# Optimization experiments

Hardware: AMD Instinct MI355X
Metric: run time of the kernel (lower is better)

The kernel has to match this reference:

```python
import jax, jax.numpy as jnp
import numpy as np

N, L = 32, 2048
C_S, C_E, C_H, K, NRES = 384, 32, 128, 7, 20
C_IN = C_S + C_E  # 416
EPS = 1e-8


def setup_inputs() -> dict:
    key = jax.random.key(0)
    ks = jax.random.split(key, 32)
    s = 0.02
    d = {}
    d['aa_seq'] = jax.random.randint(ks[0], (L,), 0, NRES)
    d['sfea_tns'] = jax.random.normal(ks[1], (N, L, C_S), jnp.float32)
    d['sfea_tns_init'] = jax.random.normal(ks[2], (N, L, C_S), jnp.float32)
    d['encd_tns'] = jax.random.normal(ks[3], (N, L, C_E), jnp.float32)
    d['quat_tns'] = jax.random.normal(ks[4], (N, L, 4), jnp.float32)
    d['trsl_tns'] = jax.random.normal(ks[5], (N, L, 3), jnp.float32)
    # FrameHead linears
    d['Wq'] = jax.random.normal(ks[6], (C_IN, 4), jnp.float32) * s
    d['bq'] = jnp.zeros((4,), jnp.float32)
    d['Wt'] = jax.random.normal(ks[7], (C_IN, 3), jnp.float32) * s
    d['bt'] = jnp.zeros((3,), jnp.float32)
    # 20 per-residue-type AngleHead experts, stacked on leading axis
    d['Wa1'] = jax.random.normal(ks[8], (NRES, C_IN, C_H), jnp.float32) * s
    d['ba1'] = jnp.zeros((NRES, C_H), jnp.float32)
    d['Wa2'] = jax.random.normal(ks[9], (NRES, C_IN, C_H), jnp.float32) * s
    d['ba2'] = jnp.zeros((NRES, C_H), jnp.float32)
    d['Wb1a'] = jax.random.normal(ks[10], (NRES, C_H, C_H), jnp.float32) * s
    d['bb1a'] = jnp.zeros((NRES, C_H), jnp.float32)
    d['Wb1b'] = jax.random.normal(ks[11], (NRES, C_H, C_H), jnp.float32) * s
    d['bb1b'] = jnp.zeros((NRES, C_H), jnp.float32)
    d['Wb2a'] = jax.random.normal(ks[12], (NRES, C_H, C_H), jnp.float32) * s
    d['bb2a'] = jnp.zeros((NRES, C_H), jnp.float32)
    d['Wb2b'] = jax.random.normal(ks[13], (NRES, C_H, C_H), jnp.float32) * s
    d['bb2b'] = jnp.zeros((NRES, C_H), jnp.float32)
    d['Wout'] = jax.random.normal(ks[14], (NRES, C_H, K * 2), jnp.float32) * s
    d['bout'] = jnp.zeros((NRES, K * 2), jnp.float32)
    return d


def _qnorm(q):
    return q * jax.lax.rsqrt(jnp.sum(q * q, -1, keepdims=True) + EPS)


def _quat_mul(q, p):
    w1, x1, y1, z1 = jnp.split(q, 4, -1)
    w2, x2, y2, z2 = jnp.split(p, 4, -1)
    return jnp.concatenate([
        w1 * w2 - x1 * x2 - y1 * y2 - z1 * z2,
        w1 * x2 + x1 * w2 + y1 * z2 - z1 * y2,
        w1 * y2 - x1 * z2 + y1 * w2 + z1 * x2,
        w1 * z2 + x1 * y2 - y1 * x2 + z1 * w2], -1)


def _quat_rotate(q, v):
    # rotate vector v by unit quaternion q = (w, xyz)
    w, qv = q[..., :1], q[..., 1:]
    t = 2.0 * jnp.cross(qv, v)
    return v + w * t + jnp.cross(qv, t)


def _angle_net(sfcd, sfcd_init, aa, Wa1, ba1, Wa2, ba2,
               Wb1a, bb1a, Wb1b, bb1b, Wb2a, bb2a, Wb2b, bb2b, Wout, bout):
    # residue-type routed AngleHead: gather each token's expert weights by aa index
    g = lambda W: jnp.take(W, aa, axis=0)  # [L, ...]
    relu = jax.nn.relu
    a = (jnp.einsum('nlc,lch->nlh', relu(sfcd), g(Wa1)) + g(ba1)
         + jnp.einsum('nlc,lch->nlh', relu(sfcd_init), g(Wa2)) + g(ba2))
    # residual block 1
    h = jnp.einsum('nlh,lhk->nlk', relu(a), g(Wb1a)) + g(bb1a)
    a = a + jnp.einsum('nlh,lhk->nlk', relu(h), g(Wb1b)) + g(bb1b)
    # residual block 2
    h = jnp.einsum('nlh,lhk->nlk', relu(a), g(Wb2a)) + g(bb2a)
    a = a + jnp.einsum('nlh,lhk->nlk', relu(h), g(Wb2b)) + g(bb2b)
    out = jnp.einsum('nlh,lhk->nlk', relu(a), g(Wout)) + g(bout)  # [N,L,2K]
    ang = out.reshape(out.shape[0], out.shape[1], K, 2)
    norm = jnp.sqrt(jnp.sum(ang * ang, -1, keepdims=True) + 1e-12)
    return ang / norm


def reference(aa_seq, sfea_tns, sfea_tns_init, encd_tns, quat_tns, trsl_tns,
              Wq, bq, Wt, bt, Wa1, ba1, Wa2, ba2, Wb1a, bb1a, Wb1b, bb1b,
              Wb2a, bb2a, Wb2b, bb2b, Wout, bout):
    sfcd = jnp.concatenate([sfea_tns, encd_tns], -1)          # [N,L,C_IN]
    sfcd_init = jnp.concatenate([sfea_tns_init, encd_tns], -1)
    # FrameHead: quaternion/translation update signals
    quat_upd = sfcd @ Wq + bq                                  # [N,L,4]
    trsl_upd = sfcd @ Wt + bt                                  # [N,L,3]
    q_old = _qnorm(quat_tns)
    quat_new = _qnorm(_quat_mul(q_old, _qnorm(quat_upd)))
    trsl_new = trsl_tns + _quat_rotate(q_old, trsl_upd)
    angl_tns = _angle_net(sfcd, sfcd_init, aa_seq, Wa1, ba1, Wa2, ba2,
                          Wb1a, bb1a, Wb1b, bb1b, Wb2a, bb2a, Wb2b, bb2b,
                          Wout, bout)
    return quat_new, trsl_new, angl_tns, quat_upd
```

## Files before the change

### kernel.cpp

```cpp
#include <hip/hip_runtime.h>

#define L_SEQ 2048
#define CS 384
#define CE 32
#define CIN 416
#define CH 128
#define NRES 20

#define ABST 136

#define PERM_BYTES 8192
#define WA_PER (CH*CIN)
#define WB_PER (CH*CH)
#define WO_PER (16*CH)
#define OFF_WA1T 0
#define OFF_WA2T (NRES*WA_PER)
#define OFF_WB1AT (2*NRES*WA_PER)
#define OFF_WB1BT (OFF_WB1AT + 1*NRES*WB_PER)
#define OFF_WB2AT (OFF_WB1AT + 2*NRES*WB_PER)
#define OFF_WB2BT (OFF_WB1AT + 3*NRES*WB_PER)
#define OFF_WOUTT (OFF_WB1AT + 4*NRES*WB_PER)
#define TOTW (OFF_WOUTT + NRES*WO_PER)
#define WS_NEED ((size_t)PERM_BYTES + (size_t)4*TOTW)

#define OUT_TR 262144
#define OUT_ANG 458752
#define OUT_QU 1376256

#define LOSCALE 4096.0f
#define ILOSCALE (1.0f/4096.0f)
#define F16MIN 6.1035156e-5f

typedef _Float16 f16x8 __attribute__((ext_vector_type(8)));
typedef _Float16 f16x4 __attribute__((ext_vector_type(4)));
typedef float f32x4 __attribute__((ext_vector_type(4)));

#define MFMA16 __builtin_amdgcn_mfma_f32_16x16x32_f16

static __device__ __forceinline__ void split1(float x, _Float16& h, _Float16& l) {
  _Float16 hi = (__builtin_fabsf(x) < F16MIN) ? (_Float16)0.f : (_Float16)x;
  h = hi;
  l = (_Float16)((x - (float)hi) * LOSCALE);
}

static __device__ __forceinline__ void split8s(const float* x, f16x8& h, f16x8& l) {
  #pragma unroll
  for (int i = 0; i < 8; ++i) { _Float16 hh, ll; split1(x[i], hh, ll); h[i] = hh; l[i] = ll; }
}

static __device__ __forceinline__ void splitrelu4(const float4& v, f16x4& h, f16x4& l) {
  const float xs[4] = {v.x, v.y, v.z, v.w};
  #pragma unroll
  for (int i = 0; i < 4; ++i) {
    const float x = fmaxf(xs[i], 0.f);
    _Float16 hh, ll; split1(x, hh, ll); h[i] = hh; l[i] = ll;
  }
}

__global__ __launch_bounds__(256) void quat_head(
    const float* __restrict__ sfea, const float* __restrict__ encd,
    const float* __restrict__ quat, const float* __restrict__ trsl,
    const float* __restrict__ Wq, const float* __restrict__ bq,
    const float* __restrict__ Wt, const float* __restrict__ bt,
    float* __restrict__ out) {
  const int wv   = threadIdx.x >> 6;
  const int lane = threadIdx.x & 63;
  const size_t idx = (size_t)blockIdx.x * 4 + wv;
  const float* __restrict__ srow = sfea + idx * CS;

  float q0=0,q1=0,q2=0,q3=0,t0=0,t1=0,t2=0;
  #pragma unroll
  for (int cc = 0; cc < 6; ++cc) {
    const int ch = cc*64 + lane;
    const float s = srow[ch];
    const float4 wq = *reinterpret_cast<const float4*>(Wq + (size_t)ch*4);
    const float* wt = Wt + (size_t)ch*3;
    q0 += s*wq.x; q1 += s*wq.y; q2 += s*wq.z; q3 += s*wq.w;
    t0 += s*wt[0]; t1 += s*wt[1]; t2 += s*wt[2];
  }
  if (lane < CE) {
    const float s = encd[idx*CE + lane];
    const int ch = CS + lane;
    const float4 wq = *reinterpret_cast<const float4*>(Wq + (size_t)ch*4);
    const float* wt = Wt + (size_t)ch*3;
    q0 += s*wq.x; q1 += s*wq.y; q2 += s*wq.z; q3 += s*wq.w;
    t0 += s*wt[0]; t1 += s*wt[1]; t2 += s*wt[2];
  }
  #pragma unroll
  for (int off = 1; off < 64; off <<= 1) {
    q0 += __shfl_xor(q0, off); q1 += __shfl_xor(q1, off);
    q2 += __shfl_xor(q2, off); q3 += __shfl_xor(q3, off);
    t0 += __shfl_xor(t0, off); t1 += __shfl_xor(t1, off);
    t2 += __shfl_xor(t2, off);
  }
  if (lane == 0) {
    const float u0 = q0 + bq[0], u1 = q1 + bq[1], u2 = q2 + bq[2], u3 = q3 + bq[3];
    const float v0 = t0 + bt[0], v1 = t1 + bt[1], v2 = t2 + bt[2];
    float a0 = quat[idx*4+0], a1 = quat[idx*4+1], a2 = quat[idx*4+2], a3 = quat[idx*4+3];
    const float rq = rsqrtf(a0*a0+a1*a1+a2*a2+a3*a3 + 1e-8f);
    a0*=rq; a1*=rq; a2*=rq; a3*=rq;
    const float ru = rsqrtf(u0*u0+u1*u1+u2*u2+u3*u3 + 1e-8f);
    const float p0=u0*ru, p1=u1*ru, p2=u2*ru, p3=u3*ru;
    const float mw = a0*p0 - a1*p1 - a2*p2 - a3*p3;
    const float mx = a0*p1 + a1*p0 + a2*p3 - a3*p2;
    const float my = a0*p2 - a1*p3 + a2*p0 + a3*p1;
    const float mz = a0*p3 + a1*p2 - a2*p1 + a3*p0;
    const float rm = rsqrtf(mw*mw+mx*mx+my*my+mz*mz + 1e-8f);
    out[idx*4+0]=mw*rm; out[idx*4+1]=mx*rm; out[idx*4+2]=my*rm; out[idx*4+3]=mz*rm;
    const float tx = 2.f*(a2*v2 - a3*v1);
    const float ty = 2.f*(a3*v0 - a1*v2);
    const float tz = 2.f*(a1*v1 - a2*v0);
    out[OUT_TR + idx*3+0] = trsl[idx*3+0] + v0 + a0*tx + (a2*tz - a3*ty);
    out[OUT_TR + idx*3+1] = trsl[idx*3+1] + v1 + a0*ty + (a3*tx - a1*tz);
    out[OUT_TR + idx*3+2] = trsl[idx*3+2] + v2 + a0*tz + (a1*ty - a2*tx);
    out[OUT_QU + idx*4+0]=u0; out[OUT_QU + idx*4+1]=u1;
    out[OUT_QU + idx*4+2]=u2; out[OUT_QU + idx*4+3]=u3;
  }
}

__global__ __launch_bounds__(1024) void build_perm(const int* __restrict__ aa_seq,
                                                   int* __restrict__ perm) {
  __shared__ int cnt[NRES*32];
  __shared__ int off[NRES*32];
  const int t = threadIdx.x;
  const int wv = t >> 6, lane = t & 63;

  int aav[2];
  #pragma unroll
  for (int h = 0; h < 2; ++h) {
    const int W = wv + h*16;
    aav[h] = aa_seq[W*64 + lane];
    #pragma unroll
    for (int a = 0; a < NRES; ++a) {
      const unsigned long long m = __ballot(aav[h] == a);
      if (lane == a) cnt[a*32 + W] = (int)__popcll(m);
    }
  }
  __syncthreads();
  if (t < 64) {
    int carry = 0;
    #pragma unroll
    for (int c = 0; c < 10; ++c) {
      const int v0 = cnt[c*64 + t];
      int v = v0;
      #pragma unroll
      for (int o = 1; o < 64; o <<= 1) {
        const int u = __shfl_up(v, o);
        if (lane >= o) v += u;
      }
      off[c*64 + t] = carry + v - v0;
      carry += __shfl(v, 63);
    }
  }
  __syncthreads();
  const unsigned long long ltmask = (lane == 0) ? 0ull : (~0ull >> (64 - lane));
  #pragma unroll
  for (int h = 0; h < 2; ++h) {
    const int W = wv + h*16;
    const int aa = aav[h];
    int pos = 0;
    #pragma unroll
    for (int a = 0; a < NRES; ++a) {
      const unsigned long long m = __ballot(aa == a);
      if (aa == a) pos = off[a*32 + W] + (int)__popcll(m & ltmask);
    }
    perm[pos] = W*64 + lane;
  }
}

__global__ __launch_bounds__(256) void convert_w(
    const float* __restrict__ Wa1, const float* __restrict__ Wa2,
    const float* __restrict__ Wb1a, const float* __restrict__ Wb1b,
    const float* __restrict__ Wb2a, const float* __restrict__ Wb2b,
    const float* __restrict__ Wout, _Float16* __restrict__ wsw) {
  const int idx = blockIdx.x * 256 + threadIdx.x;
  if (idx >= TOTW) return;
  float v;
  if (idx < OFF_WB1AT) {
    const int which = (idx < OFF_WA2T) ? 0 : 1;
    const float* W = which ? Wa2 : Wa1;
    int r = idx - which * OFF_WA2T;
    const int aa = r / WA_PER; r -= aa * WA_PER;
    const int h = r / CIN;     const int c = r - h * CIN;
    v = W[((size_t)aa*CIN + c)*CH + h];
  } else if (idx < OFF_WOUTT) {
    int q = idx - OFF_WB1AT;
    const int which = q / (NRES*WB_PER);
    int r = q - which * (NRES*WB_PER);
    const float* W = (which==0)?Wb1a:(which==1)?Wb1b:(which==2)?Wb2a:Wb2b;
    const int aa = r / WB_PER; r -= aa * WB_PER;
    const int h = r / CH;      const int c = r - h * CH;
    v = W[((size_t)aa*CH + c)*CH + h];
  } else {
    int r = idx - OFF_WOUTT;
    const int aa = r / WO_PER; r -= aa * WO_PER;
    const int kk = r / CH;     const int c = r - kk * CH;
    v = (kk < 14) ? Wout[((size_t)aa*CH + c)*14 + kk] : 0.f;
  }
  _Float16 h, l; split1(v, h, l);
  wsw[idx] = h;
  wsw[(size_t)TOTW + idx] = l;
}

static __device__ __forceinline__ void bfrag_f32(const float* __restrict__ W, int rs,
                                                 int kbase, int col, f16x8& h, f16x8& l) {
  float x[8];
  const float* p = W + (size_t)kbase * rs + col;
  #pragma unroll
  for (int j = 0; j < 8; ++j) x[j] = p[(size_t)j * rs];
  split8s(x, h, l);
}

static __device__ __forceinline__ void fold(f32x4 acc[2][2], const f32x4 accL[2][2],
                                            float b0, float b1) {
  #pragma unroll
  for (int m = 0; m < 2; ++m)
    #pragma unroll
    for (int i = 0; i < 4; ++i) {
      acc[m][0][i] += accL[m][0][i]*ILOSCALE + b0;
      acc[m][1][i] += accL[m][1][i]*ILOSCALE + b1;
    }
}

static __device__ __forceinline__ void store_relu_pair(_Float16* dh, _Float16* dl,
    const f32x4 acc[2][2], int lane, int h0) {
  const int lr = lane & 15;
  const int r0 = (lane >> 4) << 2;
  #pragma unroll
  for (int m = 0; m < 2; ++m)
    #pragma unroll
    for (int p = 0; p < 2; ++p)
      #pragma unroll
      for (int i = 0; i < 4; ++i) {
        const float v = fmaxf(acc[m][p][i], 0.f);
        _Float16 hh, ll; split1(v, hh, ll);
        const int idx = (m*16 + r0 + i)*ABST + h0 + p*16 + lr;
        dh[idx] = hh; dl[idx] = ll;
      }
}

template<bool USEWS>
static __device__ __forceinline__ void gemmA(
    const _Float16* aH, const _Float16* aL,
    const float* __restrict__ Wf, const _Float16* __restrict__ wH,
    int kbase, int nks, f32x4 acc[2][2], f32x4 accL[2][2], int lane, int h0) {
  const int lr = lane & 15;
  const int lk = (lane >> 4) << 3;
  #pragma unroll
  for (int ks = 0; ks < nks; ++ks) {
    const int kl = ks*32 + lk;
    const int kg = kbase + kl;
    const f16x8 a0h = *(const f16x8*)(aH + lr*ABST + kl);
    const f16x8 a0l = *(const f16x8*)(aL + lr*ABST + kl);
    const f16x8 a1h = *(const f16x8*)(aH + (lr+16)*ABST + kl);
    const f16x8 a1l = *(const f16x8*)(aL + (lr+16)*ABST + kl);
    f16x8 b0h, b0l, b1h, b1l;
    if constexpr (USEWS) {
      const _Float16* p0 = wH + (size_t)(h0+lr)*CIN + kg;
      const _Float16* p1 = wH + (size_t)(h0+16+lr)*CIN + kg;
      b0h = *(const f16x8*)p0; b0l = *(const f16x8*)(p0 + TOTW);
      b1h = *(const f16x8*)p1; b1l = *(const f16x8*)(p1 + TOTW);
    } else {
      bfrag_f32(Wf, CH, kg, h0+lr,    b0h, b0l);
      bfrag_f32(Wf, CH, kg, h0+16+lr, b1h, b1l);
    }
    acc [0][0] = MFMA16(a0h, b0h, acc [0][0], 0,0,0);
    accL[0][0] = MFMA16(a0h, b0l, accL[0][0], 0,0,0);
    accL[0][0] = MFMA16(a0l, b0h, accL[0][0], 0,0,0);
    acc [1][0] = MFMA16(a1h, b0h, acc [1][0], 0,0,0);
    accL[1][0] = MFMA16(a1h, b0l, accL[1][0], 0,0,0);
    accL[1][0] = MFMA16(a1l, b0h, accL[1][0], 0,0,0);
    acc [0][1] = MFMA16(a0h, b1h, acc [0][1], 0,0,0);
    accL[0][1] = MFMA16(a0h, b1l, accL[0][1], 0,0,0);
    accL[0][1] = MFMA16(a0l, b1h, accL[0][1], 0,0,0);
    acc [1][1] = MFMA16(a1h, b1h, acc [1][1], 0,0,0);
    accL[1][1] = MFMA16(a1h, b1l, accL[1][1], 0,0,0);
    accL[1][1] = MFMA16(a1l, b1h, accL[1][1], 0,0,0);
  }
}

template<bool USEWS>
static __device__ __forceinline__ void gemm128(
    const _Float16* aH, const _Float16* aL,
    const float* __restrict__ Wf, const _Float16* __restrict__ wH,
    f32x4 acc[2][2], f32x4 accL[2][2], int lane, int h0) {
  const int lr = lane & 15;
  const int lk = (lane >> 4) << 3;
  #pragma unroll
  for (int ks = 0; ks < 4; ++ks) {
    const int k = ks*32 + lk;
    const f16x8 a0h = *(const f16x8*)(aH + lr*ABST + k);
    const f16x8 a0l = *(const f16x8*)(aL + lr*ABST + k);
    const f16x8 a1h = *(const f16x8*)(aH + (lr+16)*ABST + k);
    const f16x8 a1l = *(const f16x8*)(aL + (lr+16)*ABST + k);
    f16x8 b0h, b0l, b1h, b1l;
    if constexpr (USEWS) {
      const _Float16* p0 = wH + (size_t)(h0+lr)*CH + k;
      const _Float16* p1 = wH + (size_t)(h0+16+lr)*CH + k;
      b0h = *(const f16x8*)p0; b0l = *(const f16x8*)(p0 + TOTW);
      b1h = *(const f16x8*)p1; b1l = *(const f16x8*)(p1 + TOTW);
    } else {
      bfrag_f32(Wf, CH, k, h0+lr,    b0h, b0l);
      bfrag_f32(Wf, CH, k, h0+16+lr, b1h, b1l);
    }
    acc [0][0] = MFMA16(a0h, b0h, acc [0][0], 0,0,0);
    accL[0][0] = MFMA16(a0h, b0l, accL[0][0], 0,0,0);
    accL[0][0] = MFMA16(a0l, b0h, accL[0][0], 0,0,0);
    acc [1][0] = MFMA16(a1h, b0h, acc [1][0], 0,0,0);
    accL[1][0] = MFMA16(a1h, b0l, accL[1][0], 0,0,0);
    accL[1][0] = MFMA16(a1l, b0h, accL[1][0], 0,0,0);
    acc [0][1] = MFMA16(a0h, b1h, acc [0][1], 0,0,0);
    accL[0][1] = MFMA16(a0h, b1l, accL[0][1], 0,0,0);
    accL[0][1] = MFMA16(a0l, b1h, accL[0][1], 0,0,0);
    acc [1][1] = MFMA16(a1h, b1h, acc [1][1], 0,0,0);
    accL[1][1] = MFMA16(a1h, b1l, accL[1][1], 0,0,0);
    accL[1][1] = MFMA16(a1l, b1h, accL[1][1], 0,0,0);
  }
}

template<bool USEWS>
__global__ __launch_bounds__(256, 4) void fah_main(
    const int* __restrict__ aa_seq, const int* __restrict__ perm,
    const float* __restrict__ sfea, const float* __restrict__ sfei,
    const float* __restrict__ encd,
    const float* __restrict__ Wa1, const float* __restrict__ Wa2,
    const float* __restrict__ Wb1a, const float* __restrict__ Wb1b,
    const float* __restrict__ Wb2a, const float* __restrict__ Wb2b,
    const float* __restrict__ Wout,
    const float* __restrict__ ba1, const float* __restrict__ ba2,
    const float* __restrict__ bb1a, const float* __restrict__ bb1b,
    const float* __restrict__ bb2a, const float* __restrict__ bb2b,
    const float* __restrict__ bout,
    const _Float16* __restrict__ wsw,
    float* __restrict__ out) {
  __shared__ _Float16 s1H[32*ABST], s1L[32*ABST], s2H[32*ABST], s2L[32*ABST];
  _Float16* abH = s1H;  _Float16* abL = s1L;
  _Float16* hbH = s2H;  _Float16* hbL = s2L;

  const int b  = blockIdx.x;
  const int sp = ((b & 7) << 8) | (b >> 3);
  const int l  = perm ? perm[sp] : b;
  const int t  = threadIdx.x;
  const int aa = aa_seq[l];

  const int lane = t & 63;
  const int wv   = t >> 6;
  const int lr   = lane & 15;
  const int lk   = (lane >> 4) << 3;
  const int h0   = wv * 32;

  const f32x4 zz = {0.f, 0.f, 0.f, 0.f};
  f32x4 accA[2][2], accAL[2][2];
  #pragma unroll
  for (int m = 0; m < 2; ++m) { accA[m][0]=zz; accA[m][1]=zz; accAL[m][0]=zz; accAL[m][1]=zz; }

  const float* WfA1 = Wa1 + (size_t)aa*CIN*CH;
  const float* WfA2 = Wa2 + (size_t)aa*CIN*CH;
  const _Float16* wsA1 = wsw + OFF_WA1T + (size_t)aa*WA_PER;
  const _Float16* wsA2 = wsw + OFF_WA2T + (size_t)aa*WA_PER;

  const int n  = t >> 3;
  const int sj = t & 7;
  #pragma unroll
  for (int ck = 0; ck < 4; ++ck) {
    const int koff = ck * 128;
    if (ck < 3) {
      const float* srow = sfea + ((size_t)n*L_SEQ + l)*CS + koff;
      const float* irow = sfei + ((size_t)n*L_SEQ + l)*CS + koff;
      #pragma unroll
      for (int u = 0; u < 4; ++u) {
        const int c = sj*16 + u*4;
        f16x4 h4, l4;
        splitrelu4(*reinterpret_cast<const float4*>(srow + c), h4, l4);
        *(f16x4*)(s1H + n*ABST + c) = h4;  *(f16x4*)(s1L + n*ABST + c) = l4;
        splitrelu4(*reinterpret_cast<const float4*>(irow + c), h4, l4);
        *(f16x4*)(s2H + n*ABST + c) = h4;  *(f16x4*)(s2L + n*ABST + c) = l4;
      }
    } else {
      const float* erow = encd + ((size_t)n*L_SEQ + l)*CE;
      const int c = sj*4;
      f16x4 h4, l4;
      splitrelu4(*reinterpret_cast<const float4*>(erow + c), h4, l4);
      *(f16x4*)(s1H + n*ABST + c) = h4;  *(f16x4*)(s1L + n*ABST + c) = l4;
      *(f16x4*)(s2H + n*ABST + c) = h4;  *(f16x4*)(s2L + n*ABST + c) = l4;
    }
    __syncthreads();
    const int nks = (ck < 3) ? 4 : 1;
    gemmA<USEWS>(s1H, s1L, WfA1, wsA1, koff, nks, accA, accAL, lane, h0);
    gemmA<USEWS>(s2H, s2L, WfA2, wsA2, koff, nks, accA, accAL, lane, h0);
    __syncthreads();
  }
  fold(accA, accAL,
       ba1[aa*CH + h0 + lr]      + ba2[aa*CH + h0 + lr],
       ba1[aa*CH + h0 + 16 + lr] + ba2[aa*CH + h0 + 16 + lr]);
  store_relu_pair(abH, abL, accA, lane, h0);
  __syncthreads();

  {
    f32x4 acc[2][2], accL[2][2];
    #pragma unroll
    for (int m = 0; m < 2; ++m) { acc[m][0]=zz; acc[m][1]=zz; accL[m][0]=zz; accL[m][1]=zz; }
    gemm128<USEWS>(abH, abL, Wb1a + (size_t)aa*WB_PER,
                   wsw + OFF_WB1AT + (size_t)aa*WB_PER, acc, accL, lane, h0);
    fold(acc, accL, bb1a[aa*CH + h0 + lr], bb1a[aa*CH + h0 + 16 + lr]);
    store_relu_pair(hbH, hbL, acc, lane, h0);
  }
  __syncthreads();
  {
    f32x4 accL[2][2];
    #pragma unroll
    for (int m = 0; m < 2; ++m) { accL[m][0]=zz; accL[m][1]=zz; }
    gemm128<USEWS>(hbH, hbL, Wb1b + (size_t)aa*WB_PER,
                   wsw + OFF_WB1BT + (size_t)aa*WB_PER, accA, accL, lane, h0);
    fold(accA, accL, bb1b[aa*CH + h0 + lr], bb1b[aa*CH + h0 + 16 + lr]);
    store_relu_pair(abH, abL, accA, lane, h0);
  }
  __syncthreads();
  {
    f32x4 acc[2][2], accL[2][2];
    #pragma unroll
    for (int m = 0; m < 2; ++m) { acc[m][0]=zz; acc[m][1]=zz; accL[m][0]=zz; accL[m][1]=zz; }
    gemm128<USEWS>(abH, abL, Wb2a + (size_t)aa*WB_PER,
                   wsw + OFF_WB2AT + (size_t)aa*WB_PER, acc, accL, lane, h0);
    fold(acc, accL, bb2a[aa*CH + h0 + lr], bb2a[aa*CH + h0 + 16 + lr]);
    store_relu_pair(hbH, hbL, acc, lane, h0);
  }
  __syncthreads();
  {
    f32x4 accL[2][2];
    #pragma unroll
    for (int m = 0; m < 2; ++m) { accL[m][0]=zz; accL[m][1]=zz; }
    gemm128<USEWS>(hbH, hbL, Wb2b + (size_t)aa*WB_PER,
                   wsw + OFF_WB2BT + (size_t)aa*WB_PER, accA, accL, lane, h0);
    fold(accA, accL, bb2b[aa*CH + h0 + lr], bb2b[aa*CH + h0 + 16 + lr]);
    store_relu_pair(abH, abL, accA, lane, h0);
  }
  __syncthreads();

  if (wv < 2) {
    f32x4 o = zz, oL = zz;
    #pragma unroll
    for (int ks = 0; ks < 4; ++ks) {
      const int k = ks*32 + lk;
      const f16x8 ah = *(const f16x8*)(abH + (wv*16 + lr)*ABST + k);
      const f16x8 al = *(const f16x8*)(abL + (wv*16 + lr)*ABST + k);
      f16x8 bh, bl;
      if constexpr (USEWS) {
        const _Float16* p = wsw + OFF_WOUTT + (size_t)aa*WO_PER + (size_t)lr*CH + k;
        bh = *(const f16x8*)p; bl = *(const f16x8*)(p + TOTW);
      } else {
        if (lr < 14) {
          bfrag_f32(Wout + (size_t)aa*CH*14, 14, k, lr, bh, bl);
        } else {
          #pragma unroll
          for (int j = 0; j < 8; ++j) { bh[j] = (_Float16)0.f; bl[j] = (_Float16)0.f; }
        }
      }
      o  = MFMA16(ah, bh, o,  0,0,0);
      oL = MFMA16(ah, bl, oL, 0,0,0);
      oL = MFMA16(al, bh, oL, 0,0,0);
    }
    const float bo = (lr < 14) ? bout[aa*14 + lr] : 0.f;
    #pragma unroll
    for (int i = 0; i < 4; ++i) {
      const float v  = o[i] + oL[i]*ILOSCALE + bo;
      const float pv = __shfl_xor(v, 1);
      const float r  = rsqrtf(v*v + pv*pv + 1e-12f);
      if (lr < 14) {
        const int nrow = wv*16 + ((lane >> 4) << 2) + i;
        out[OUT_ANG + (size_t)nrow*(L_SEQ*14) + (size_t)l*14 + lr] = v*r;
      }
    }
  }
}

extern "C" void kernel_launch(void* const* d_in, const int* in_sizes, int n_in,
                              void* d_out, int out_size, void* d_ws, size_t ws_size,
                              hipStream_t stream) {
  const int*   aa   = (const int*)  d_in[0];
  const float* sfea = (const float*)d_in[1];
  const float* sfei = (const float*)d_in[2];
  const float* encd = (const float*)d_in[3];
  const float* quat = (const float*)d_in[4];
  const float* trsl = (const float*)d_in[5];
  const float* Wq   = (const float*)d_in[6];
  const float* bq   = (const float*)d_in[7];
  const float* Wt   = (const float*)d_in[8];
  const float* bt   = (const float*)d_in[9];
  const float* Wa1  = (const float*)d_in[10];
  const float* ba1  = (const float*)d_in[11];
  const float* Wa2  = (const float*)d_in[12];
  const float* ba2  = (const float*)d_in[13];
  const float* Wb1a = (const float*)d_in[14];
  const float* bb1a = (const float*)d_in[15];
  const float* Wb1b = (const float*)d_in[16];
  const float* bb1b = (const float*)d_in[17];
  const float* Wb2a = (const float*)d_in[18];
  const float* bb2a = (const float*)d_in[19];
  const float* Wb2b = (const float*)d_in[20];
  const float* bb2b = (const float*)d_in[21];
  const float* Wout = (const float*)d_in[22];
  const float* bout = (const float*)d_in[23];
  float* out = (float*)d_out;

  const bool useperm = ws_size >= (size_t)PERM_BYTES;
  const bool usews   = ws_size >= WS_NEED;
  int* perm = useperm ? (int*)d_ws : nullptr;
  _Float16* wsw = (_Float16*)((char*)d_ws + PERM_BYTES);

  if (useperm)
    hipLaunchKernelGGL(build_perm, dim3(1), dim3(1024), 0, stream, aa, perm);
  if (usews)
    hipLaunchKernelGGL(convert_w, dim3((TOTW + 255)/256), dim3(256), 0, stream,
                       Wa1, Wa2, Wb1a, Wb1b, Wb2a, Wb2b, Wout, wsw);
  hipLaunchKernelGGL(quat_head, dim3(16384), dim3(256), 0, stream,
                     sfea, encd, quat, trsl, Wq, bq, Wt, bt, out);
  if (usews)
    hipLaunchKernelGGL((fah_main<true>), dim3(L_SEQ), dim3(256), 0, stream,
                       aa, perm, sfea, sfei, encd,
                       Wa1, Wa2, Wb1a, Wb1b, Wb2a, Wb2b, Wout,
                       ba1, ba2, bb1a, bb1b, bb2a, bb2b, bout, wsw, out);
  else
    hipLaunchKernelGGL((fah_main<false>), dim3(L_SEQ), dim3(256), 0, stream,
                       aa, perm, sfea, sfei, encd,
                       Wa1, Wa2, Wb1a, Wb1b, Wb2a, Wb2b, Wout,
                       ba1, ba2, bb1a, bb1b, bb2a, bb2b, bout, wsw, out);
}
```

Before: 219.3 us.

## Process two same-residue positions per block to reuse expert weight fragments

The permutation is rebuilt with each residue-type group padded to even length (stored as u16), so every block handles two sequence positions sharing an expert. Each weight B-fragment loaded from the converted fp16 hi/lo workspace now feeds MFMAs for both positions, halving weight traffic per position, and the grid shrinks to 1034 blocks with a custom XCD-aware mapping. The fallback path for missing workspace is removed, occupancy hint drops to 2 blocks/SM with doubled LDS and register use, and padded duplicate positions redo work and rewrite identical outputs.

```diff
diff --git a/kernel.cpp b/kernel.cpp
--- a/kernel.cpp
+++ b/kernel.cpp
@@ -8,8 +8,10 @@
 #define NRES 20
 
 #define ABST 136
-
-#define PERM_BYTES 8192
+#define PADN 2068
+#define NB2  1034
+
+#define PERM_REGION 4608
 #define WA_PER (CH*CIN)
 #define WB_PER (CH*CH)
 #define WO_PER (16*CH)
@@ -21,7 +23,6 @@
 #define OFF_WB2BT (OFF_WB1AT + 3*NRES*WB_PER)
 #define OFF_WOUTT (OFF_WB1AT + 4*NRES*WB_PER)
 #define TOTW (OFF_WOUTT + NRES*WO_PER)
-#define WS_NEED ((size_t)PERM_BYTES + (size_t)4*TOTW)
 
 #define OUT_TR 262144
 #define OUT_ANG 458752
@@ -41,20 +42,6 @@
   _Float16 hi = (__builtin_fabsf(x) < F16MIN) ? (_Float16)0.f : (_Float16)x;
   h = hi;
   l = (_Float16)((x - (float)hi) * LOSCALE);
-}
-
-static __device__ __forceinline__ void split8s(const float* x, f16x8& h, f16x8& l) {
-  #pragma unroll
-  for (int i = 0; i < 8; ++i) { _Float16 hh, ll; split1(x[i], hh, ll); h[i] = hh; l[i] = ll; }
-}
-
-static __device__ __forceinline__ void splitrelu4(const float4& v, f16x4& h, f16x4& l) {
-  const float xs[4] = {v.x, v.y, v.z, v.w};
-  #pragma unroll
-  for (int i = 0; i < 4; ++i) {
-    const float x = fmaxf(xs[i], 0.f);
-    _Float16 hh, ll; split1(x, hh, ll); h[i] = hh; l[i] = ll;
-  }
 }
 
 __global__ __launch_bounds__(256) void quat_head(
@@ -119,11 +106,15 @@
 }
 
 __global__ __launch_bounds__(1024) void build_perm(const int* __restrict__ aa_seq,
-                                                   int* __restrict__ perm) {
+                                                   unsigned short* __restrict__ perm) {
   __shared__ int cnt[NRES*32];
-  __shared__ int off[NRES*32];
+  __shared__ int woff[NRES*32];
+  __shared__ int poff_s[NRES];
+  __shared__ int ctot_s[NRES];
   const int t = threadIdx.x;
   const int wv = t >> 6, lane = t & 63;
+
+  for (int i = t; i < PADN; i += 1024) perm[i] = 0;
 
   int aav[2];
   #pragma unroll
@@ -137,19 +128,29 @@
     }
   }
   __syncthreads();
-  if (t < 64) {
-    int carry = 0;
-    #pragma unroll
-    for (int c = 0; c < 10; ++c) {
-      const int v0 = cnt[c*64 + t];
+  if (t < 32) {
+    int tot = 0;
+    if (t < NRES) {
+      #pragma unroll
+      for (int W = 0; W < 32; ++W) tot += cnt[t*32 + W];
+    }
+    const int pa = (t < NRES) ? ((tot + 1) & ~1) : 0;
+    int s = pa;
+    #pragma unroll
+    for (int o = 1; o < 32; o <<= 1) {
+      const int u = __shfl_up(s, o);
+      if (lane >= o) s += u;
+    }
+    if (t < NRES) { poff_s[t] = s - pa; ctot_s[t] = tot; }
+    for (int a = 0; a < NRES; ++a) {
+      const int v0 = cnt[a*32 + t];
       int v = v0;
       #pragma unroll
-      for (int o = 1; o < 64; o <<= 1) {
+      for (int o = 1; o < 32; o <<= 1) {
         const int u = __shfl_up(v, o);
         if (lane >= o) v += u;
       }
-      off[c*64 + t] = carry + v - v0;
-      carry += __shfl(v, 63);
+      woff[a*32 + t] = poff_s[a] + v - v0;
     }
   }
   __syncthreads();
@@ -157,14 +158,16 @@
   #pragma unroll
   for (int h = 0; h < 2; ++h) {
     const int W = wv + h*16;
-    const int aa = aav[h];
+    const int a = aav[h];
     int pos = 0;
     #pragma unroll
-    for (int a = 0; a < NRES; ++a) {
-      const unsigned long long m = __ballot(aa == a);
-      if (aa == a) pos = off[a*32 + W] + (int)__popcll(m & ltmask);
-    }
-    perm[pos] = W*64 + lane;
+    for (int aq = 0; aq < NRES; ++aq) {
+      const unsigned long long m = __ballot(a == aq);
+      if (a == aq) pos = woff[aq*32 + W] + (int)__popcll(m & ltmask);
+    }
+    const unsigned short lv = (unsigned short)(W*64 + lane);
+    perm[pos] = lv;
+    if ((ctot_s[a] & 1) && pos == poff_s[a] + ctot_s[a] - 1) perm[pos + 1] = lv;
   }
 }
 
@@ -202,15 +205,6 @@
   wsw[(size_t)TOTW + idx] = l;
 }
 
-static __device__ __forceinline__ void bfrag_f32(const float* __restrict__ W, int rs,
-                                                 int kbase, int col, f16x8& h, f16x8& l) {
-  float x[8];
-  const float* p = W + (size_t)kbase * rs + col;
-  #pragma unroll
-  for (int j = 0; j < 8; ++j) x[j] = p[(size_t)j * rs];
-  split8s(x, h, l);
-}
-
 static __device__ __forceinline__ void fold(f32x4 acc[2][2], const f32x4 accL[2][2],
                                             float b0, float b1) {
   #pragma unroll
@@ -239,223 +233,221 @@
       }
 }
 
-template<bool USEWS>
-static __device__ __forceinline__ void gemmA(
-    const _Float16* aH, const _Float16* aL,
-    const float* __restrict__ Wf, const _Float16* __restrict__ wH,
-    int kbase, int nks, f32x4 acc[2][2], f32x4 accL[2][2], int lane, int h0) {
+template<int S>
+static __device__ __forceinline__ void gemm_dual(
+    const _Float16* aH0, const _Float16* aL0,
+    const _Float16* aH1, const _Float16* aL1,
+    const _Float16* __restrict__ wH,
+    int kbase, int nks,
+    f32x4 acc0[2][2], f32x4 acc0L[2][2],
+    f32x4 acc1[2][2], f32x4 acc1L[2][2],
+    int lane, int h0) {
   const int lr = lane & 15;
   const int lk = (lane >> 4) << 3;
   #pragma unroll
   for (int ks = 0; ks < nks; ++ks) {
     const int kl = ks*32 + lk;
     const int kg = kbase + kl;
-    const f16x8 a0h = *(const f16x8*)(aH + lr*ABST + kl);
-    const f16x8 a0l = *(const f16x8*)(aL + lr*ABST + kl);
-    const f16x8 a1h = *(const f16x8*)(aH + (lr+16)*ABST + kl);
-    const f16x8 a1l = *(const f16x8*)(aL + (lr+16)*ABST + kl);
-    f16x8 b0h, b0l, b1h, b1l;
-    if constexpr (USEWS) {
-      const _Float16* p0 = wH + (size_t)(h0+lr)*CIN + kg;
-      const _Float16* p1 = wH + (size_t)(h0+16+lr)*CIN + kg;
-      b0h = *(const f16x8*)p0; b0l = *(const f16x8*)(p0 + TOTW);
-      b1h = *(const f16x8*)p1; b1l = *(const f16x8*)(p1 + TOTW);
-    } else {
-      bfrag_f32(Wf, CH, kg, h0+lr,    b0h, b0l);
-      bfrag_f32(Wf, CH, kg, h0+16+lr, b1h, b1l);
-    }
-    acc [0][0] = MFMA16(a0h, b0h, acc [0][0], 0,0,0);
-    accL[0][0] = MFMA16(a0h, b0l, accL[0][0], 0,0,0);
-    accL[0][0] = MFMA16(a0l, b0h, accL[0][0], 0,0,0);
-    acc [1][0] = MFMA16(a1h, b0h, acc [1][0], 0,0,0);
-    accL[1][0] = MFMA16(a1h, b0l, accL[1][0], 0,0,0);
-    accL[1][0] = MFMA16(a1l, b0h, accL[1][0], 0,0,0);
-    acc [0][1] = MFMA16(a0h, b1h, acc [0][1], 0,0,0);
-    accL[0][1] = MFMA16(a0h, b1l, accL[0][1], 0,0,0);
-    accL[0][1] = MFMA16(a0l, b1h, accL[0][1], 0,0,0);
-    acc [1][1] = MFMA16(a1h, b1h, acc [1][1], 0,0,0);
-    accL[1][1] = MFMA16(a1h, b1l, accL[1][1], 0,0,0);
-    accL[1][1] = MFMA16(a1l, b1h, accL[1][1], 0,0,0);
-  }
-}
-
-template<bool USEWS>
-static __device__ __forceinline__ void gemm128(
-    const _Float16* aH, const _Float16* aL,
-    const float* __restrict__ Wf, const _Float16* __restrict__ wH,
-    f32x4 acc[2][2], f32x4 accL[2][2], int lane, int h0) {
-  const int lr = lane & 15;
-  const int lk = (lane >> 4) << 3;
-  #pragma unroll
-  for (int ks = 0; ks < 4; ++ks) {
-    const int k = ks*32 + lk;
-    const f16x8 a0h = *(const f16x8*)(aH + lr*ABST + k);
-    const f16x8 a0l = *(const f16x8*)(aL + lr*ABST + k);
-    const f16x8 a1h = *(const f16x8*)(aH + (lr+16)*ABST + k);
-    const f16x8 a1l = *(const f16x8*)(aL + (lr+16)*ABST + k);
-    f16x8 b0h, b0l, b1h, b1l;
-    if constexpr (USEWS) {
-      const _Float16* p0 = wH + (size_t)(h0+lr)*CH + k;
-      const _Float16* p1 = wH + (size_t)(h0+16+lr)*CH + k;
-      b0h = *(const f16x8*)p0; b0l = *(const f16x8*)(p0 + TOTW);
-      b1h = *(const f16x8*)p1; b1l = *(const f16x8*)(p1 + TOTW);
-    } else {
-      bfrag_f32(Wf, CH, k, h0+lr,    b0h, b0l);
-      bfrag_f32(Wf, CH, k, h0+16+lr, b1h, b1l);
-    }
-    acc [0][0] = MFMA16(a0h, b0h, acc [0][0], 0,0,0);
-    accL[0][0] = MFMA16(a0h, b0l, accL[0][0], 0,0,0);
-    accL[0][0] = MFMA16(a0l, b0h, accL[0][0], 0,0,0);
-    acc [1][0] = MFMA16(a1h, b0h, acc [1][0], 0,0,0);
-    accL[1][0] = MFMA16(a1h, b0l, accL[1][0], 0,0,0);
-    accL[1][0] = MFMA16(a1l, b0h, accL[1][0], 0,0,0);
-    acc [0][1] = MFMA16(a0h, b1h, acc [0][1], 0,0,0);
-    accL[0][1] = MFMA16(a0h, b1l, accL[0][1], 0,0,0);
-    accL[0][1] = MFMA16(a0l, b1h, accL[0][1], 0,0,0);
-    acc [1][1] = MFMA16(a1h, b1h, acc [1][1], 0,0,0);
-    accL[1][1] = MFMA16(a1h, b1l, accL[1][1], 0,0,0);
-    accL[1][1] = MFMA16(a1l, b1h, accL[1][1], 0,0,0);
-  }
-}
-
-template<bool USEWS>
-__global__ __launch_bounds__(256, 4) void fah_main(
-    const int* __restrict__ aa_seq, const int* __restrict__ perm,
+    const _Float16* p0 = wH + (size_t)(h0+lr)*S + kg;
+    const _Float16* p1 = wH + (size_t)(h0+16+lr)*S + kg;
+    const f16x8 b0h = *(const f16x8*)p0;
+    const f16x8 b0l = *(const f16x8*)(p0 + TOTW);
+    const f16x8 b1h = *(const f16x8*)p1;
+    const f16x8 b1l = *(const f16x8*)(p1 + TOTW);
+#define DOPOS(AH, AL, AC, ACL) { \
+    const f16x8 a0h = *(const f16x8*)(AH + lr*ABST + kl); \
+    const f16x8 a0l = *(const f16x8*)(AL + lr*ABST + kl); \
+    const f16x8 a1h = *(const f16x8*)(AH + (lr+16)*ABST + kl); \
+    const f16x8 a1l = *(const f16x8*)(AL + (lr+16)*ABST + kl); \
+    AC[0][0]  = MFMA16(a0h, b0h, AC[0][0], 0,0,0); \
+    ACL[0][0] = MFMA16(a0h, b0l, ACL[0][0], 0,0,0); \
+    ACL[0][0] = MFMA16(a0l, b0h, ACL[0][0], 0,0,0); \
+    AC[1][0]  = MFMA16(a1h, b0h, AC[1][0], 0,0,0); \
+    ACL[1][0] = MFMA16(a1h, b0l, ACL[1][0], 0,0,0); \
+    ACL[1][0] = MFMA16(a1l, b0h, ACL[1][0], 0,0,0); \
+    AC[0][1]  = MFMA16(a0h, b1h, AC[0][1], 0,0,0); \
+    ACL[0][1] = MFMA16(a0h, b1l, ACL[0][1], 0,0,0); \
+    ACL[0][1] = MFMA16(a0l, b1h, ACL[0][1], 0,0,0); \
+    AC[1][1]  = MFMA16(a1h, b1h, AC[1][1], 0,0,0); \
+    ACL[1][1] = MFMA16(a1h, b1l, ACL[1][1], 0,0,0); \
+    ACL[1][1] = MFMA16(a1l, b1h, ACL[1][1], 0,0,0); }
+    DOPOS(aH0, aL0, acc0, acc0L)
+    DOPOS(aH1, aL1, acc1, acc1L)
+#undef DOPOS
+  }
+}
+
+static __device__ __forceinline__ void stage_row128(
+    const float* __restrict__ row, _Float16* dH, _Float16* dL, int n, int sj) {
+  #pragma unroll
+  for (int q2 = 0; q2 < 2; ++q2) {
+    const int cl = q2*64 + sj*8;
+    const float4 v0 = *(const float4*)(row + cl);
+    const float4 v1 = *(const float4*)(row + cl + 4);
+    const float xs[8] = {v0.x,v0.y,v0.z,v0.w,v1.x,v1.y,v1.z,v1.w};
+    f16x8 h8, l8;
+    #pragma unroll
+    for (int e = 0; e < 8; ++e) {
+      _Float16 hh, ll; split1(fmaxf(xs[e], 0.f), hh, ll);
+      h8[e] = hh; l8[e] = ll;
+    }
+    *(f16x8*)(dH + n*ABST + cl) = h8;
+    *(f16x8*)(dL + n*ABST + cl) = l8;
+  }
+}
+
+static __device__ __forceinline__ void stage_encd(
+    const float* __restrict__ erow,
+    _Float16* sH, _Float16* sL, _Float16* iH, _Float16* iL, int n, int sj) {
+  const int cl = sj*4;
+  const float4 v = *(const float4*)(erow + cl);
+  const float xs[4] = {v.x, v.y, v.z, v.w};
+  f16x4 h4, l4;
+  #pragma unroll
+  for (int e = 0; e < 4; ++e) {
+    _Float16 hh, ll; split1(fmaxf(xs[e], 0.f), hh, ll);
+    h4[e] = hh; l4[e] = ll;
+  }
+  *(f16x4*)(sH + n*ABST + cl) = h4;  *(f16x4*)(sL + n*ABST + cl) = l4;
+  *(f16x4*)(iH + n*ABST + cl) = h4;  *(f16x4*)(iL + n*ABST + cl) = l4;
+}
+
+__global__ __launch_bounds__(256, 2) void fah_main(
+    const int* __restrict__ aa_seq, const unsigned short* __restrict__ perm,
     const float* __restrict__ sfea, const float* __restrict__ sfei,
     const float* __restrict__ encd,
-    const float* __restrict__ Wa1, const float* __restrict__ Wa2,
-    const float* __restrict__ Wb1a, const float* __restrict__ Wb1b,
-    const float* __restrict__ Wb2a, const float* __restrict__ Wb2b,
-    const float* __restrict__ Wout,
     const float* __restrict__ ba1, const float* __restrict__ ba2,
     const float* __restrict__ bb1a, const float* __restrict__ bb1b,
     const float* __restrict__ bb2a, const float* __restrict__ bb2b,
     const float* __restrict__ bout,
     const _Float16* __restrict__ wsw,
     float* __restrict__ out) {
-  __shared__ _Float16 s1H[32*ABST], s1L[32*ABST], s2H[32*ABST], s2L[32*ABST];
-  _Float16* abH = s1H;  _Float16* abL = s1L;
-  _Float16* hbH = s2H;  _Float16* hbL = s2L;
-
-  const int b  = blockIdx.x;
-  const int sp = ((b & 7) << 8) | (b >> 3);
-  const int l  = perm ? perm[sp] : b;
-  const int t  = threadIdx.x;
-  const int aa = aa_seq[l];
-
-  const int lane = t & 63;
-  const int wv   = t >> 6;
-  const int lr   = lane & 15;
-  const int lk   = (lane >> 4) << 3;
-  const int h0   = wv * 32;
+  __shared__ __align__(16) _Float16 sf0H[32*ABST], sf0L[32*ABST];
+  __shared__ __align__(16) _Float16 in0H[32*ABST], in0L[32*ABST];
+  __shared__ __align__(16) _Float16 sf1H[32*ABST], sf1L[32*ABST];
+  __shared__ __align__(16) _Float16 in1H[32*ABST], in1L[32*ABST];
+  _Float16 *ab0H = sf0H, *ab0L = sf0L, *hb0H = in0H, *hb0L = in0L;
+  _Float16 *ab1H = sf1H, *ab1L = sf1L, *hb1H = in1H, *hb1L = in1L;
+
+  const int orig = blockIdx.x;
+  const int xcd = orig & 7, i8 = orig >> 3;
+  const int sp = (xcd < 2 ? xcd*130 : 260 + (xcd-2)*129) + i8;
+  const int l0 = perm[2*sp], l1 = perm[2*sp+1];
+  const int aa = aa_seq[l0];
+
+  const int t = threadIdx.x;
+  const int lane = t & 63, wv = t >> 6;
+  const int lr = lane & 15, lk = (lane >> 4) << 3, h0 = wv * 32;
+  const int n = t >> 3, sj = t & 7;
 
   const f32x4 zz = {0.f, 0.f, 0.f, 0.f};
-  f32x4 accA[2][2], accAL[2][2];
-  #pragma unroll
-  for (int m = 0; m < 2; ++m) { accA[m][0]=zz; accA[m][1]=zz; accAL[m][0]=zz; accAL[m][1]=zz; }
-
-  const float* WfA1 = Wa1 + (size_t)aa*CIN*CH;
-  const float* WfA2 = Wa2 + (size_t)aa*CIN*CH;
+  f32x4 accA0[2][2], accA0L[2][2], accA1[2][2], accA1L[2][2];
+  #pragma unroll
+  for (int m = 0; m < 2; ++m) {
+    accA0[m][0]=zz; accA0[m][1]=zz; accA0L[m][0]=zz; accA0L[m][1]=zz;
+    accA1[m][0]=zz; accA1[m][1]=zz; accA1L[m][0]=zz; accA1L[m][1]=zz;
+  }
+
   const _Float16* wsA1 = wsw + OFF_WA1T + (size_t)aa*WA_PER;
   const _Float16* wsA2 = wsw + OFF_WA2T + (size_t)aa*WA_PER;
 
-  const int n  = t >> 3;
-  const int sj = t & 7;
   #pragma unroll
   for (int ck = 0; ck < 4; ++ck) {
     const int koff = ck * 128;
     if (ck < 3) {
-      const float* srow = sfea + ((size_t)n*L_SEQ + l)*CS + koff;
-      const float* irow = sfei + ((size_t)n*L_SEQ + l)*CS + koff;
-      #pragma unroll
-      for (int u = 0; u < 4; ++u) {
-        const int c = sj*16 + u*4;
-        f16x4 h4, l4;
-        splitrelu4(*reinterpret_cast<const float4*>(srow + c), h4, l4);
-        *(f16x4*)(s1H + n*ABST + c) = h4;  *(f16x4*)(s1L + n*ABST + c) = l4;
-        splitrelu4(*reinterpret_cast<const float4*>(irow + c), h4, l4);
-        *(f16x4*)(s2H + n*ABST + c) = h4;  *(f16x4*)(s2L + n*ABST + c) = l4;
-      }
+      stage_row128(sfea + ((size_t)n*L_SEQ + l0)*CS + koff, sf0H, sf0L, n, sj);
+      stage_row128(sfei + ((size_t)n*L_SEQ + l0)*CS + koff, in0H, in0L, n, sj);
+      stage_row128(sfea + ((size_t)n*L_SEQ + l1)*CS + koff, sf1H, sf1L, n, sj);
+      stage_row128(sfei + ((size_t)n*L_SEQ + l1)*CS + koff, in1H, in1L, n, sj);
     } else {
-      const float* erow = encd + ((size_t)n*L_SEQ + l)*CE;
-      const int c = sj*4;
-      f16x4 h4, l4;
-      splitrelu4(*reinterpret_cast<const float4*>(erow + c), h4, l4);
-      *(f16x4*)(s1H + n*ABST + c) = h4;  *(f16x4*)(s1L + n*ABST + c) = l4;
-      *(f16x4*)(s2H + n*ABST + c) = h4;  *(f16x4*)(s2L + n*ABST + c) = l4;
+      stage_encd(encd + ((size_t)n*L_SEQ + l0)*CE, sf0H, sf0L, in0H, in0L, n, sj);
+      stage_encd(encd + ((size_t)n*L_SEQ + l1)*CE, sf1H, sf1L, in1H, in1L, n, sj);
     }
     __syncthreads();
     const int nks = (ck < 3) ? 4 : 1;
-    gemmA<USEWS>(s1H, s1L, WfA1, wsA1, koff, nks, accA, accAL, lane, h0);
-    gemmA<USEWS>(s2H, s2L, WfA2, wsA2, koff, nks, accA, accAL, lane, h0);
+    gemm_dual<CIN>(sf0H, sf0L, sf1H, sf1L, wsA1, koff, nks,
+                   accA0, accA0L, accA1, accA1L, lane, h0);
+    gemm_dual<CIN>(in0H, in0L, in1H, in1L, wsA2, koff, nks,
+                   accA0, accA0L, accA1, accA1L, lane, h0);
     __syncthreads();
   }
-  fold(accA, accAL,
-       ba1[aa*CH + h0 + lr]      + ba2[aa*CH + h0 + lr],
-       ba1[aa*CH + h0 + 16 + lr] + ba2[aa*CH + h0 + 16 + lr]);
-  store_relu_pair(abH, abL, accA, lane, h0);
-  __syncthreads();
 
   {
-    f32x4 acc[2][2], accL[2][2];
-    #pragma unroll
-    for (int m = 0; m < 2; ++m) { acc[m][0]=zz; acc[m][1]=zz; accL[m][0]=zz; accL[m][1]=zz; }
-    gemm128<USEWS>(abH, abL, Wb1a + (size_t)aa*WB_PER,
-                   wsw + OFF_WB1AT + (size_t)aa*WB_PER, acc, accL, lane, h0);
-    fold(acc, accL, bb1a[aa*CH + h0 + lr], bb1a[aa*CH + h0 + 16 + lr]);
-    store_relu_pair(hbH, hbL, acc, lane, h0);
-  }
-  __syncthreads();
+    const float b0v = ba1[aa*CH + h0 + lr]      + ba2[aa*CH + h0 + lr];
+    const float b1v = ba1[aa*CH + h0 + 16 + lr] + ba2[aa*CH + h0 + 16 + lr];
+    fold(accA0, accA0L, b0v, b1v);
+    fold(accA1, accA1L, b0v, b1v);
+    store_relu_pair(ab0H, ab0L, accA0, lane, h0);
+    store_relu_pair(ab1H, ab1L, accA1, lane, h0);
+  }
+  __syncthreads();
+
   {
-    f32x4 accL[2][2];
-    #pragma unroll
-    for (int m = 0; m < 2; ++m) { accL[m][0]=zz; accL[m][1]=zz; }
-    gemm128<USEWS>(hbH, hbL, Wb1b + (size_t)aa*WB_PER,
-                   wsw + OFF_WB1BT + (size_t)aa*WB_PER, accA, accL, lane, h0);
-    fold(accA, accL, bb1b[aa*CH + h0 + lr], bb1b[aa*CH + h0 + 16 + lr]);
-    store_relu_pair(abH, abL, accA, lane, h0);
+    f32x4 c0[2][2], c0L[2][2], c1[2][2], c1L[2][2];
+    #pragma unroll
+    for (int m = 0; m < 2; ++m) { c0[m][0]=zz;c0[m][1]=zz;c0L[m][0]=zz;c0L[m][1]=zz;
+                                  c1[m][0]=zz;c1[m][1]=zz;c1L[m][0]=zz;c1L[m][1]=zz; }
+    gemm_dual<CH>(ab0H, ab0L, ab1H, ab1L, wsw + OFF_WB1AT + (size_t)aa*WB_PER, 0, 4,
+                  c0, c0L, c1, c1L, lane, h0);
+    const float B0 = bb1a[aa*CH + h0 + lr], B1 = bb1a[aa*CH + h0 + 16 + lr];
+    fold(c0, c0L, B0, B1); fold(c1, c1L, B0, B1);
+    store_relu_pair(hb0H, hb0L, c0, lane, h0);
+    store_relu_pair(hb1H, hb1L, c1, lane, h0);
   }
   __syncthreads();
   {
-    f32x4 acc[2][2], accL[2][2];
-    #pragma unroll
-    for (int m = 0; m < 2; ++m) { acc[m][0]=zz; acc[m][1]=zz; accL[m][0]=zz; accL[m][1]=zz; }
-    gemm128<USEWS>(abH, abL, Wb2a + (size_t)aa*WB_PER,
-                   wsw + OFF_WB2AT + (size_t)aa*WB_PER, acc, accL, lane, h0);
-    fold(acc, accL, bb2a[aa*CH + h0 + lr], bb2a[aa*CH + h0 + 16 + lr]);
-    store_relu_pair(hbH, hbL, acc, lane, h0);
+    f32x4 c0L[2][2], c1L[2][2];
+    #pragma unroll
+    for (int m = 0; m < 2; ++m) { c0L[m][0]=zz;c0L[m][1]=zz;c1L[m][0]=zz;c1L[m][1]=zz; }
+    gemm_dual<CH>(hb0H, hb0L, hb1H, hb1L, wsw + OFF_WB1BT + (size_t)aa*WB_PER, 0, 4,
+                  accA0, c0L, accA1, c1L, lane, h0);
+    const float B0 = bb1b[aa*CH + h0 + lr], B1 = bb1b[aa*CH + h0 + 16 + lr];
+    fold(accA0, c0L, B0, B1); fold(accA1, c1L, B0, B1);
+    store_relu_pair(ab0H, ab0L, accA0, lane, h0);
+    store_relu_pair(ab1H, ab1L, accA1, lane, h0);
   }
   __syncthreads();
   {
-    f32x4 accL[2][2];
-    #pragma unroll
-    for (int m = 0; m < 2; ++m) { accL[m][0]=zz; accL[m][1]=zz; }
-    gemm128<USEWS>(hbH, hbL, Wb2b + (size_t)aa*WB_PER,
-                   wsw + OFF_WB2BT + (size_t)aa*WB_PER, accA, accL, lane, h0);
-    fold(accA, accL, bb2b[aa*CH + h0 + lr], bb2b[aa*CH + h0 + 16 + lr]);
-    store_relu_pair(abH, abL, accA, lane, h0);
-  }
-  __syncthreads();
-
-  if (wv < 2) {
+    f32x4 c0[2][2], c0L[2][2], c1[2][2], c1L[2][2];
+    #pragma unroll
+    for (int m = 0; m < 2; ++m) { c0[m][0]=zz;c0[m][1]=zz;c0L[m][0]=zz;c0L[m][1]=zz;
+                                  c1[m][0]=zz;c1[m][1]=zz;c1L[m][0]=zz;c1L[m][1]=zz; }
+    gemm_dual<CH>(ab0H, ab0L, ab1H, ab1L, wsw + OFF_WB2AT + (size_t)aa*WB_PER, 0, 4,
+                  c0, c0L, c1, c1L, lane, h0);
+    const float B0 = bb2a[aa*CH + h0 + lr], B1 = bb2a[aa*CH + h0 + 16 + lr];
+    fold(c0, c0L, B0, B1); fold(c1, c1L, B0, B1);
+    store_relu_pair(hb0H, hb0L, c0, lane, h0);
+    store_relu_pair(hb1H, hb1L, c1, lane, h0);
+  }
+  __syncthreads();
+  {
+    f32x4 c0L[2][2], c1L[2][2];
+    #pragma unroll
+    for (int m = 0; m < 2; ++m) { c0L[m][0]=zz;c0L[m][1]=zz;c1L[m][0]=zz;c1L[m][1]=zz; }
+    gemm_dual<CH>(hb0H, hb0L, hb1H, hb1L, wsw + OFF_WB2BT + (size_t)aa*WB_PER, 0, 4,
+                  accA0, c0L, accA1, c1L, lane, h0);
+    const float B0 = bb2b[aa*CH + h0 + lr], B1 = bb2b[aa*CH + h0 + 16 + lr];
+    fold(accA0, c0L, B0, B1); fold(accA1, c1L, B0, B1);
+    store_relu_pair(ab0H, ab0L, accA0, lane, h0);
+    store_relu_pair(ab1H, ab1L, accA1, lane, h0);
+  }
+  __syncthreads();
+
+  {
+    const int pos  = wv >> 1;
+    const int half = wv & 1;
+    const _Float16* aH = pos ? ab1H : ab0H;
+    const _Float16* aL = pos ? ab1L : ab0L;
+    const int lsel = pos ? l1 : l0;
     f32x4 o = zz, oL = zz;
     #pragma unroll
     for (int ks = 0; ks < 4; ++ks) {
       const int k = ks*32 + lk;
-      const f16x8 ah = *(const f16x8*)(abH + (wv*16 + lr)*ABST + k);
-      const f16x8 al = *(const f16x8*)(abL + (wv*16 + lr)*ABST + k);
-      f16x8 bh, bl;
-      if constexpr (USEWS) {
-        const _Float16* p = wsw + OFF_WOUTT + (size_t)aa*WO_PER + (size_t)lr*CH + k;
-        bh = *(const f16x8*)p; bl = *(const f16x8*)(p + TOTW);
-      } else {
-        if (lr < 14) {
-          bfrag_f32(Wout + (size_t)aa*CH*14, 14, k, lr, bh, bl);
-        } else {
-          #pragma unroll
-          for (int j = 0; j < 8; ++j) { bh[j] = (_Float16)0.f; bl[j] = (_Float16)0.f; }
-        }
-      }
+      const f16x8 ah = *(const f16x8*)(aH + (half*16 + lr)*ABST + k);
+      const f16x8 al = *(const f16x8*)(aL + (half*16 + lr)*ABST + k);
+      const _Float16* p = wsw + OFF_WOUTT + (size_t)aa*WO_PER + (size_t)lr*CH + k;
+      const f16x8 bh = *(const f16x8*)p;
+      const f16x8 bl = *(const f16x8*)(p + TOTW);
       o  = MFMA16(ah, bh, o,  0,0,0);
       oL = MFMA16(ah, bl, oL, 0,0,0);
       oL = MFMA16(al, bh, oL, 0,0,0);
@@ -467,8 +459,8 @@
       const float pv = __shfl_xor(v, 1);
       const float r  = rsqrtf(v*v + pv*pv + 1e-12f);
       if (lr < 14) {
-        const int nrow = wv*16 + ((lane >> 4) << 2) + i;
-        out[OUT_ANG + (size_t)nrow*(L_SEQ*14) + (size_t)l*14 + lr] = v*r;
+        const int nrow = half*16 + ((lane >> 4) << 2) + i;
+        out[OUT_ANG + (size_t)nrow*(L_SEQ*14) + (size_t)lsel*14 + lr] = v*r;
       }
     }
   }
@@ -503,26 +495,15 @@
   const float* bout = (const float*)d_in[23];
   float* out = (float*)d_out;
 
-  const bool useperm = ws_size >= (size_t)PERM_BYTES;
-  const bool usews   = ws_size >= WS_NEED;
-  int* perm = useperm ? (int*)d_ws : nullptr;
-  _Float16* wsw = (_Float16*)((char*)d_ws + PERM_BYTES);
-
-  if (useperm)
-    hipLaunchKernelGGL(build_perm, dim3(1), dim3(1024), 0, stream, aa, perm);
-  if (usews)
-    hipLaunchKernelGGL(convert_w, dim3((TOTW + 255)/256), dim3(256), 0, stream,
-                       Wa1, Wa2, Wb1a, Wb1b, Wb2a, Wb2b, Wout, wsw);
+  unsigned short* perm = (unsigned short*)d_ws;
+  _Float16* wsw = (_Float16*)((char*)d_ws + PERM_REGION);
+
+  hipLaunchKernelGGL(build_perm, dim3(1), dim3(1024), 0, stream, aa, perm);
+  hipLaunchKernelGGL(convert_w, dim3((TOTW + 255)/256), dim3(256), 0, stream,
+                     Wa1, Wa2, Wb1a, Wb1b, Wb2a, Wb2b, Wout, wsw);
   hipLaunchKernelGGL(quat_head, dim3(16384), dim3(256), 0, stream,
                      sfea, encd, quat, trsl, Wq, bq, Wt, bt, out);
-  if (usews)
-    hipLaunchKernelGGL((fah_main<true>), dim3(L_SEQ), dim3(256), 0, stream,
-                       aa, perm, sfea, sfei, encd,
-                       Wa1, Wa2, Wb1a, Wb1b, Wb2a, Wb2b, Wout,
-                       ba1, ba2, bb1a, bb1b, bb2a, bb2b, bout, wsw, out);
-  else
-    hipLaunchKernelGGL((fah_main<false>), dim3(L_SEQ), dim3(256), 0, stream,
-                       aa, perm, sfea, sfei, encd,
-                       Wa1, Wa2, Wb1a, Wb1b, Wb2a, Wb2b, Wout,
-                       ba1, ba2, bb1a, bb1b, bb2a, bb2b, bout, wsw, out);
-}
+  hipLaunchKernelGGL(fah_main, dim3(NB2), dim3(256), 0, stream,
+                     aa, perm, sfea, sfei, encd,
+                     ba1, ba2, bb1a, bb1b, bb2a, bb2b, bout, wsw, out);
+}
```

Result: faster. 209.2 us (-4.6%).
